# Kernel optimization log

Hardware: AMD Instinct MI355X
Metric: run time of the kernel (lower is better)

The kernel has to match this reference:

```python
import jax, jax.numpy as jnp
import numpy as np

B, T, Q, D = 8192, 65, 20, 100  # batch, tweet len, question len, 2*hidden_dim


def setup_inputs() -> dict:
    key = jax.random.key(0)
    kH, kU, k1, k2, k3 = jax.random.split(key, 5)
    # Ws params are a single normal row repeated across the length dim
    ws1 = jnp.tile(jax.random.normal(k1, (1, D), dtype=jnp.float32), (T, 1))
    ws2 = jnp.tile(jax.random.normal(k2, (1, D), dtype=jnp.float32), (Q, 1))
    ws3 = jnp.tile(jax.random.normal(k3, (1, D), dtype=jnp.float32), (T, 1))
    return {
        "H": jax.random.normal(kH, (B, T, D), dtype=jnp.float32),
        "U": jax.random.normal(kU, (B, Q, D), dtype=jnp.float32),
        "Ws1": ws1,
        "Ws2": ws2,
        "Ws3": ws3,
    }


def reference(H, U, Ws1, Ws2, Ws3):
    # H: [B,T,D], U: [B,Q,D]
    H1 = jnp.sum(H * Ws1, axis=2)[:, :, None]        # [B,T,1]
    U1 = jnp.sum(U * Ws2, axis=2)[:, None, :]        # [B,1,Q]
    HU = jnp.einsum('btd,bqd->btq', H * Ws3, U)      # [B,T,Q]
    S = H1 + U1 + HU                                 # [B,T,Q]
    at = jax.nn.softmax(S, axis=2)                   # attend tweet->question
    Util = jnp.einsum('btq,bqd->btd', at, U)         # [B,T,D]
    beta = jnp.max(S, axis=2)                        # [B,T]
    b = jax.nn.softmax(beta, axis=1)[:, :, None]     # [B,T,1]
    Htil = jnp.sum(b * H, axis=1)[:, None, :]        # [B,1,D] broadcast over T
    G = jnp.concatenate((H, Util, H * Util, H * Htil), axis=2)  # [B,T,4D]
    return G
```

## Files before the change

### kernel.cpp

```cpp
#include <hip/hip_runtime.h>
#include <math.h>

#define NB 8192
#define T 65
#define Q 20
#define D 100
#define D4 25
#define C 21
#define SP 24

__global__ __launch_bounds__(256) void attn_fused_kernel(
    const float* __restrict__ Hg,
    const float* __restrict__ Ug,
    const float* __restrict__ Ws1,
    const float* __restrict__ Ws2,
    const float* __restrict__ Ws3,
    float* __restrict__ Gg)
{
    __shared__ __align__(16) float sH[T*D];
    __shared__ __align__(16) float sU[Q*D];
    __shared__ __align__(16) float sU3e[C*D];
    __shared__ __align__(16) float sS[T*SP];
    __shared__ __align__(16) float sHtil[D];
    __shared__ float sU1q[Q];
    __shared__ float sBeta[T];
    __shared__ float sBsm[T];

    const int b   = blockIdx.x;
    const int tid = threadIdx.x;
    const float* Hb = Hg + (size_t)b * (T*D);
    const float* Ub = Ug + (size_t)b * (Q*D);
    float4* sH4   = (float4*)sH;
    float4* sU4   = (float4*)sU;
    float4* sU3e4 = (float4*)sU3e;
    float4* sS4   = (float4*)sS;

    {
        const float4* hs = (const float4*)Hb;
        for (int i = tid; i < T*D4; i += 256) sH4[i] = hs[i];
        const float4* us = (const float4*)Ub;
        for (int i = tid; i < Q*D4; i += 256) sU4[i] = us[i];
    }
    __syncthreads();

    {
        const float4* w3g = (const float4*)Ws3;
        const float4* w1g = (const float4*)Ws1;
        for (int i = tid; i < C*D4; i += 256) {
            const int r  = i / D4;
            const int dd = i - r*D4;
            float4 v;
            if (r < Q) {
                const float4 u = sU4[i];
                const float4 w = w3g[dd];
                v.x = u.x*w.x; v.y = u.y*w.y; v.z = u.z*w.z; v.w = u.w*w.w;
            } else {
                v = w1g[dd];
            }
            sU3e4[i] = v;
        }
        if (tid < Q) {
            const float4* ur = sU4 + tid*D4;
            const float4* w2 = (const float4*)Ws2;
            float acc = 0.f;
            #pragma unroll
            for (int k = 0; k < D4; ++k) {
                const float4 u = ur[k], w = w2[k];
                acc = fmaf(u.x, w.x, acc); acc = fmaf(u.y, w.y, acc);
                acc = fmaf(u.z, w.z, acc); acc = fmaf(u.w, w.w, acc);
            }
            sU1q[tid] = acc;
        }
    }
    __syncthreads();

    if (tid < 119) {
        const int tg = tid / 7;
        const int jg = tid - tg*7;
        const int t0 = tg*4;
        float acc[4][3];
        #pragma unroll
        for (int i = 0; i < 4; ++i)
            #pragma unroll
            for (int k = 0; k < 3; ++k) acc[i][k] = 0.f;
        #pragma unroll 5
        for (int d4 = 0; d4 < D4; ++d4) {
            float4 h[4];
            #pragma unroll
            for (int i = 0; i < 4; ++i) h[i] = sH4[(t0+i)*D4 + d4];
            #pragma unroll
            for (int k = 0; k < 3; ++k) {
                const float4 w = sU3e4[(jg*3+k)*D4 + d4];
                #pragma unroll
                for (int i = 0; i < 4; ++i) {
                    acc[i][k] = fmaf(h[i].x, w.x, acc[i][k]);
                    acc[i][k] = fmaf(h[i].y, w.y, acc[i][k]);
                    acc[i][k] = fmaf(h[i].z, w.z, acc[i][k]);
                    acc[i][k] = fmaf(h[i].w, w.w, acc[i][k]);
                }
            }
        }
        #pragma unroll
        for (int i = 0; i < 4; ++i) {
            const int t = t0 + i;
            if (t < T) {
                #pragma unroll
                for (int k = 0; k < 3; ++k) {
                    const int cc = jg*3 + k;
                    const float add = (cc < Q) ? sU1q[cc] : 0.f;
                    sS[t*SP + cc] = acc[i][k] + add;
                }
            }
        }
    }
    __syncthreads();

    if (tid < T) {
        const int t = tid;
        float4 r[5];
        #pragma unroll
        for (int c = 0; c < 5; ++c) r[c] = sS4[t*6 + c];
        const float h1t = sS[t*SP + 20];
        float m = r[0].x;
        #pragma unroll
        for (int c = 0; c < 5; ++c) {
            m = fmaxf(m, fmaxf(fmaxf(r[c].x, r[c].y), fmaxf(r[c].z, r[c].w)));
        }
        float s = 0.f;
        #pragma unroll
        for (int c = 0; c < 5; ++c) {
            r[c].x = __expf(r[c].x - m); r[c].y = __expf(r[c].y - m);
            r[c].z = __expf(r[c].z - m); r[c].w = __expf(r[c].w - m);
            s += r[c].x + r[c].y + r[c].z + r[c].w;
        }
        const float inv = 1.f / s;
        #pragma unroll
        for (int c = 0; c < 5; ++c) {
            r[c].x *= inv; r[c].y *= inv; r[c].z *= inv; r[c].w *= inv;
            sS4[t*6 + c] = r[c];
        }
        sBeta[t] = h1t + m;
    }
    __syncthreads();

    if (tid < 64) {
        const float v0 = sBeta[tid];
        const float v1 = (tid == 0) ? sBeta[64] : -1e30f;
        float mx = fmaxf(v0, v1);
        #pragma unroll
        for (int off = 32; off >= 1; off >>= 1)
            mx = fmaxf(mx, __shfl_xor(mx, off, 64));
        const float e0 = __expf(v0 - mx);
        const float e1 = (tid == 0) ? __expf(v1 - mx) : 0.f;
        float s = e0 + e1;
        #pragma unroll
        for (int off = 32; off >= 1; off >>= 1)
            s += __shfl_xor(s, off, 64);
        const float inv = 1.f / s;
        sBsm[tid] = e0 * inv;
        if (tid == 0) sBsm[64] = e1 * inv;
    }
    __syncthreads();

    if (tid < D4) {
        float4 acc = {0.f, 0.f, 0.f, 0.f};
        #pragma unroll 5
        for (int t = 0; t < T; ++t) {
            const float bt = sBsm[t];
            const float4 h = sH4[t*D4 + tid];
            acc.x = fmaf(bt, h.x, acc.x); acc.y = fmaf(bt, h.y, acc.y);
            acc.z = fmaf(bt, h.z, acc.z); acc.w = fmaf(bt, h.w, acc.w);
        }
        ((float4*)sHtil)[tid] = acc;
    }
    __syncthreads();

    {
        const int wv   = tid >> 6;
        const int lane = tid & 63;
        const int tsel = lane / 25;
        const int g    = lane - tsel*25;
        const bool act = (lane < 50);
        float* Gb = Gg + (size_t)b * (T*4*D);
        const float4 htil4 = ((float4*)sHtil)[g];
        const float4* ug = sU4 + g;

        for (int pr = wv; pr < 33; pr += 4) {
            const int t   = pr*2 + tsel;
            const bool val = act && (t < T);
            const int tr  = val ? t : 0;

            float4 a0 = sS4[tr*6 + 0];
            float4 a1 = sS4[tr*6 + 1];
            float4 a2 = sS4[tr*6 + 2];
            float4 a3 = sS4[tr*6 + 3];
            float4 a4 = sS4[tr*6 + 4];

            float4 acc = {0.f, 0.f, 0.f, 0.f};
            #define QSTEP(av, comp, qq) { \
                const float4 u = ug[(qq)*D4]; \
                acc.x = fmaf(av.comp, u.x, acc.x); \
                acc.y = fmaf(av.comp, u.y, acc.y); \
                acc.z = fmaf(av.comp, u.z, acc.z); \
                acc.w = fmaf(av.comp, u.w, acc.w); }
            QSTEP(a0,x,0)  QSTEP(a0,y,1)  QSTEP(a0,z,2)  QSTEP(a0,w,3)
            QSTEP(a1,x,4)  QSTEP(a1,y,5)  QSTEP(a1,z,6)  QSTEP(a1,w,7)
            QSTEP(a2,x,8)  QSTEP(a2,y,9)  QSTEP(a2,z,10) QSTEP(a2,w,11)
            QSTEP(a3,x,12) QSTEP(a3,y,13) QSTEP(a3,z,14) QSTEP(a3,w,15)
            QSTEP(a4,x,16) QSTEP(a4,y,17) QSTEP(a4,z,18) QSTEP(a4,w,19)
            #undef QSTEP

            const float4 h4 = sH4[tr*D4 + g];
            if (val) {
                float* base = Gb + (size_t)t*(4*D);
                float4 hu, hh;
                hu.x = h4.x*acc.x;   hu.y = h4.y*acc.y;   hu.z = h4.z*acc.z;   hu.w = h4.w*acc.w;
                hh.x = h4.x*htil4.x; hh.y = h4.y*htil4.y; hh.z = h4.z*htil4.z; hh.w = h4.w*htil4.w;
                ((float4*)(base        ))[g] = h4;
                ((float4*)(base +   D  ))[g] = acc;
                ((float4*)(base + 2*D  ))[g] = hu;
                ((float4*)(base + 3*D  ))[g] = hh;
            }
        }
    }
}

extern "C" void kernel_launch(void* const* d_in, const int* in_sizes, int n_in,
                              void* d_out, int out_size, void* d_ws, size_t ws_size,
                              hipStream_t stream) {
    const float* H   = (const float*)d_in[0];
    const float* U   = (const float*)d_in[1];
    const float* Ws1 = (const float*)d_in[2];
    const float* Ws2 = (const float*)d_in[3];
    const float* Ws3 = (const float*)d_in[4];
    float* G = (float*)d_out;
    hipLaunchKernelGGL(attn_fused_kernel, dim3(NB), dim3(256), 0, stream,
                       H, U, Ws1, Ws2, Ws3, G);
}
```

Before: 320.8 us.

## Retile S-GEMM and Util phases, split Htil across waves, fuse U loads

The per-thread tile in the score GEMM grows from 4x3 to 8x3, and the U1 dot products move onto a separate wave so they run alongside it. Htil is reduced with all four waves through partial sums. The Util phase handles three rows per thread so each U load is reused. The U copy and the Ws3 scaling are fused into one global pass, which removes one barrier, and launch bounds now request 3 blocks per CU. The larger tiles raise register pressure, and the occupancy hint could cause spills.

```diff
diff --git a/kernel.cpp b/kernel.cpp
--- a/kernel.cpp
+++ b/kernel.cpp
@@ -6,10 +6,9 @@
 #define Q 20
 #define D 100
 #define D4 25
-#define C 21
-#define SP 24
-
-__global__ __launch_bounds__(256) void attn_fused_kernel(
+#define SP4 5
+
+__global__ __launch_bounds__(256, 3) void attn_fused_kernel(
     const float* __restrict__ Hg,
     const float* __restrict__ Ug,
     const float* __restrict__ Ws1,
@@ -17,129 +16,122 @@
     const float* __restrict__ Ws3,
     float* __restrict__ Gg)
 {
-    __shared__ __align__(16) float sH[T*D];
-    __shared__ __align__(16) float sU[Q*D];
-    __shared__ __align__(16) float sU3e[C*D];
-    __shared__ __align__(16) float sS[T*SP];
-    __shared__ __align__(16) float sHtil[D];
-    __shared__ float sU1q[Q];
-    __shared__ float sBeta[T];
-    __shared__ float sBsm[T];
+    __shared__ float4 sH4[T*D4];
+    __shared__ float4 sU4[Q*D4];
+    __shared__ float4 sU3e4[(Q+1)*D4];
+    __shared__ float4 sS4[T*SP4];
+    __shared__ float4 sHtilP[4][D4];
+    __shared__ float4 sU1q4[SP4];
+    __shared__ float  sH1[T];
+    __shared__ float  sBeta[T];
+    __shared__ float  sBsm[T];
 
     const int b   = blockIdx.x;
     const int tid = threadIdx.x;
-    const float* Hb = Hg + (size_t)b * (T*D);
-    const float* Ub = Ug + (size_t)b * (Q*D);
-    float4* sH4   = (float4*)sH;
-    float4* sU4   = (float4*)sU;
-    float4* sU3e4 = (float4*)sU3e;
-    float4* sS4   = (float4*)sS;
-
-    {
-        const float4* hs = (const float4*)Hb;
-        for (int i = tid; i < T*D4; i += 256) sH4[i] = hs[i];
-        const float4* us = (const float4*)Ub;
-        for (int i = tid; i < Q*D4; i += 256) sU4[i] = us[i];
-    }
-    __syncthreads();
-
+    const float4* Hb = (const float4*)(Hg + (size_t)b * (T*D));
+    const float4* Ub = (const float4*)(Ug + (size_t)b * (Q*D));
+
+    for (int i = tid; i < T*D4; i += 256) sH4[i] = Hb[i];
     {
         const float4* w3g = (const float4*)Ws3;
-        const float4* w1g = (const float4*)Ws1;
-        for (int i = tid; i < C*D4; i += 256) {
-            const int r  = i / D4;
-            const int dd = i - r*D4;
-            float4 v;
-            if (r < Q) {
-                const float4 u = sU4[i];
-                const float4 w = w3g[dd];
-                v.x = u.x*w.x; v.y = u.y*w.y; v.z = u.z*w.z; v.w = u.w*w.w;
-            } else {
-                v = w1g[dd];
-            }
+        for (int i = tid; i < Q*D4; i += 256) {
+            const float4 u = Ub[i];
+            sU4[i] = u;
+            const int dd = i - (i/D4)*D4;
+            const float4 w = w3g[dd];
+            float4 v; v.x=u.x*w.x; v.y=u.y*w.y; v.z=u.z*w.z; v.w=u.w*w.w;
             sU3e4[i] = v;
         }
-        if (tid < Q) {
-            const float4* ur = sU4 + tid*D4;
-            const float4* w2 = (const float4*)Ws2;
-            float acc = 0.f;
-            #pragma unroll
-            for (int k = 0; k < D4; ++k) {
-                const float4 u = ur[k], w = w2[k];
-                acc = fmaf(u.x, w.x, acc); acc = fmaf(u.y, w.y, acc);
-                acc = fmaf(u.z, w.z, acc); acc = fmaf(u.w, w.w, acc);
-            }
-            sU1q[tid] = acc;
-        }
-    }
-    __syncthreads();
-
-    if (tid < 119) {
+        if (tid < D4) sU3e4[Q*D4 + tid] = ((const float4*)Ws1)[tid];
+    }
+    __syncthreads();
+
+    if (tid < 63) {
         const int tg = tid / 7;
         const int jg = tid - tg*7;
-        const int t0 = tg*4;
-        float acc[4][3];
-        #pragma unroll
-        for (int i = 0; i < 4; ++i)
+        int tb[8];
+        #pragma unroll
+        for (int i = 0; i < 8; ++i) {
+            const int t = tg*8 + i;
+            tb[i] = ((t < T) ? t : T-1) * D4;
+        }
+        float acc[8][3];
+        #pragma unroll
+        for (int i = 0; i < 8; ++i)
             #pragma unroll
             for (int k = 0; k < 3; ++k) acc[i][k] = 0.f;
         #pragma unroll 5
         for (int d4 = 0; d4 < D4; ++d4) {
-            float4 h[4];
-            #pragma unroll
-            for (int i = 0; i < 4; ++i) h[i] = sH4[(t0+i)*D4 + d4];
-            #pragma unroll
-            for (int k = 0; k < 3; ++k) {
-                const float4 w = sU3e4[(jg*3+k)*D4 + d4];
+            float4 w[3];
+            #pragma unroll
+            for (int k = 0; k < 3; ++k) w[k] = sU3e4[(jg*3+k)*D4 + d4];
+            #pragma unroll
+            for (int i = 0; i < 8; ++i) {
+                const float4 h = sH4[tb[i] + d4];
                 #pragma unroll
-                for (int i = 0; i < 4; ++i) {
-                    acc[i][k] = fmaf(h[i].x, w.x, acc[i][k]);
-                    acc[i][k] = fmaf(h[i].y, w.y, acc[i][k]);
-                    acc[i][k] = fmaf(h[i].z, w.z, acc[i][k]);
-                    acc[i][k] = fmaf(h[i].w, w.w, acc[i][k]);
+                for (int k = 0; k < 3; ++k) {
+                    acc[i][k] = fmaf(h.x, w[k].x, acc[i][k]);
+                    acc[i][k] = fmaf(h.y, w[k].y, acc[i][k]);
+                    acc[i][k] = fmaf(h.z, w[k].z, acc[i][k]);
+                    acc[i][k] = fmaf(h.w, w[k].w, acc[i][k]);
                 }
             }
         }
-        #pragma unroll
-        for (int i = 0; i < 4; ++i) {
-            const int t = t0 + i;
+        float* sSf = (float*)sS4;
+        #pragma unroll
+        for (int i = 0; i < 8; ++i) {
+            const int t = tg*8 + i;
             if (t < T) {
                 #pragma unroll
                 for (int k = 0; k < 3; ++k) {
                     const int cc = jg*3 + k;
-                    const float add = (cc < Q) ? sU1q[cc] : 0.f;
-                    sS[t*SP + cc] = acc[i][k] + add;
+                    if (cc < Q) sSf[t*(4*SP4) + cc] = acc[i][k];
+                    else        sH1[t] = acc[i][k];
                 }
             }
         }
+    } else if (tid >= 64 && tid < 64 + Q) {
+        const int q = tid - 64;
+        const float4* ur = sU4 + q*D4;
+        const float4* w2 = (const float4*)Ws2;
+        float acc = 0.f;
+        #pragma unroll
+        for (int k = 0; k < D4; ++k) {
+            const float4 u = ur[k], w = w2[k];
+            acc = fmaf(u.x, w.x, acc); acc = fmaf(u.y, w.y, acc);
+            acc = fmaf(u.z, w.z, acc); acc = fmaf(u.w, w.w, acc);
+        }
+        ((float*)sU1q4)[q] = acc;
     }
     __syncthreads();
 
     if (tid < T) {
         const int t = tid;
-        float4 r[5];
-        #pragma unroll
-        for (int c = 0; c < 5; ++c) r[c] = sS4[t*6 + c];
-        const float h1t = sS[t*SP + 20];
+        float4 r[SP4];
+        #pragma unroll
+        for (int c = 0; c < SP4; ++c) {
+            r[c] = sS4[t*SP4 + c];
+            const float4 u1 = sU1q4[c];
+            r[c].x += u1.x; r[c].y += u1.y; r[c].z += u1.z; r[c].w += u1.w;
+        }
         float m = r[0].x;
         #pragma unroll
-        for (int c = 0; c < 5; ++c) {
+        for (int c = 0; c < SP4; ++c)
             m = fmaxf(m, fmaxf(fmaxf(r[c].x, r[c].y), fmaxf(r[c].z, r[c].w)));
-        }
         float s = 0.f;
         #pragma unroll
-        for (int c = 0; c < 5; ++c) {
+        for (int c = 0; c < SP4; ++c) {
             r[c].x = __expf(r[c].x - m); r[c].y = __expf(r[c].y - m);
             r[c].z = __expf(r[c].z - m); r[c].w = __expf(r[c].w - m);
             s += r[c].x + r[c].y + r[c].z + r[c].w;
         }
         const float inv = 1.f / s;
         #pragma unroll
-        for (int c = 0; c < 5; ++c) {
+        for (int c = 0; c < SP4; ++c) {
             r[c].x *= inv; r[c].y *= inv; r[c].z *= inv; r[c].w *= inv;
-            sS4[t*6 + c] = r[c];
-        }
-        sBeta[t] = h1t + m;
+            sS4[t*SP4 + c] = r[c];
+        }
+        sBeta[t] = sH1[t] + m;
     }
     __syncthreads();
 
@@ -162,16 +154,18 @@
     }
     __syncthreads();
 
-    if (tid < D4) {
-        float4 acc = {0.f, 0.f, 0.f, 0.f};
-        #pragma unroll 5
-        for (int t = 0; t < T; ++t) {
-            const float bt = sBsm[t];
-            const float4 h = sH4[t*D4 + tid];
-            acc.x = fmaf(bt, h.x, acc.x); acc.y = fmaf(bt, h.y, acc.y);
-            acc.z = fmaf(bt, h.z, acc.z); acc.w = fmaf(bt, h.w, acc.w);
-        }
-        ((float4*)sHtil)[tid] = acc;
+    {
+        const int wv = tid >> 6, lane = tid & 63;
+        if (lane < D4) {
+            float4 acc = {0.f, 0.f, 0.f, 0.f};
+            for (int t = wv; t < T; t += 4) {
+                const float bt = sBsm[t];
+                const float4 h = sH4[t*D4 + lane];
+                acc.x = fmaf(bt, h.x, acc.x); acc.y = fmaf(bt, h.y, acc.y);
+                acc.z = fmaf(bt, h.z, acc.z); acc.w = fmaf(bt, h.w, acc.w);
+            }
+            sHtilP[wv][lane] = acc;
+        }
     }
     __syncthreads();
 
@@ -182,45 +176,62 @@
         const int g    = lane - tsel*25;
         const bool act = (lane < 50);
         float* Gb = Gg + (size_t)b * (T*4*D);
-        const float4 htil4 = ((float4*)sHtil)[g];
-        const float4* ug = sU4 + g;
-
-        for (int pr = wv; pr < 33; pr += 4) {
-            const int t   = pr*2 + tsel;
-            const bool val = act && (t < T);
-            const int tr  = val ? t : 0;
-
-            float4 a0 = sS4[tr*6 + 0];
-            float4 a1 = sS4[tr*6 + 1];
-            float4 a2 = sS4[tr*6 + 2];
-            float4 a3 = sS4[tr*6 + 3];
-            float4 a4 = sS4[tr*6 + 4];
-
-            float4 acc = {0.f, 0.f, 0.f, 0.f};
-            #define QSTEP(av, comp, qq) { \
-                const float4 u = ug[(qq)*D4]; \
-                acc.x = fmaf(av.comp, u.x, acc.x); \
-                acc.y = fmaf(av.comp, u.y, acc.y); \
-                acc.z = fmaf(av.comp, u.z, acc.z); \
-                acc.w = fmaf(av.comp, u.w, acc.w); }
-            QSTEP(a0,x,0)  QSTEP(a0,y,1)  QSTEP(a0,z,2)  QSTEP(a0,w,3)
-            QSTEP(a1,x,4)  QSTEP(a1,y,5)  QSTEP(a1,z,6)  QSTEP(a1,w,7)
-            QSTEP(a2,x,8)  QSTEP(a2,y,9)  QSTEP(a2,z,10) QSTEP(a2,w,11)
-            QSTEP(a3,x,12) QSTEP(a3,y,13) QSTEP(a3,z,14) QSTEP(a3,w,15)
-            QSTEP(a4,x,16) QSTEP(a4,y,17) QSTEP(a4,z,18) QSTEP(a4,w,19)
-            #undef QSTEP
-
-            const float4 h4 = sH4[tr*D4 + g];
-            if (val) {
-                float* base = Gb + (size_t)t*(4*D);
-                float4 hu, hh;
-                hu.x = h4.x*acc.x;   hu.y = h4.y*acc.y;   hu.z = h4.z*acc.z;   hu.w = h4.w*acc.w;
-                hh.x = h4.x*htil4.x; hh.y = h4.y*htil4.y; hh.z = h4.z*htil4.z; hh.w = h4.w*htil4.w;
-                ((float4*)(base        ))[g] = h4;
-                ((float4*)(base +   D  ))[g] = acc;
-                ((float4*)(base + 2*D  ))[g] = hu;
-                ((float4*)(base + 3*D  ))[g] = hh;
-            }
+
+        const float4 p0 = sHtilP[0][g], p1 = sHtilP[1][g], p2 = sHtilP[2][g], p3 = sHtilP[3][g];
+        float4 htil;
+        htil.x = p0.x+p1.x+p2.x+p3.x; htil.y = p0.y+p1.y+p2.y+p3.y;
+        htil.z = p0.z+p1.z+p2.z+p3.z; htil.w = p0.w+p1.w+p2.w+p3.w;
+
+        for (int c = wv; c < 11; c += 4) {
+            const int t0 = c*6 + tsel;
+            int tr0 = (t0     < T) ? t0     : T-1;
+            int tr1 = (t0 + 2 < T) ? t0 + 2 : T-1;
+            int tr2 = (t0 + 4 < T) ? t0 + 4 : T-1;
+            float4 a0[SP4], a1[SP4], a2[SP4];
+            #pragma unroll
+            for (int j = 0; j < SP4; ++j) {
+                a0[j] = sS4[tr0*SP4 + j];
+                a1[j] = sS4[tr1*SP4 + j];
+                a2[j] = sS4[tr2*SP4 + j];
+            }
+            float4 c0 = {0,0,0,0}, c1 = {0,0,0,0}, c2 = {0,0,0,0};
+            #define QST(qq, comp) { \
+                const float4 u = sU4[(qq)*D4 + g]; \
+                c0.x = fmaf(a0[(qq)>>2].comp, u.x, c0.x); \
+                c0.y = fmaf(a0[(qq)>>2].comp, u.y, c0.y); \
+                c0.z = fmaf(a0[(qq)>>2].comp, u.z, c0.z); \
+                c0.w = fmaf(a0[(qq)>>2].comp, u.w, c0.w); \
+                c1.x = fmaf(a1[(qq)>>2].comp, u.x, c1.x); \
+                c1.y = fmaf(a1[(qq)>>2].comp, u.y, c1.y); \
+                c1.z = fmaf(a1[(qq)>>2].comp, u.z, c1.z); \
+                c1.w = fmaf(a1[(qq)>>2].comp, u.w, c1.w); \
+                c2.x = fmaf(a2[(qq)>>2].comp, u.x, c2.x); \
+                c2.y = fmaf(a2[(qq)>>2].comp, u.y, c2.y); \
+                c2.z = fmaf(a2[(qq)>>2].comp, u.z, c2.z); \
+                c2.w = fmaf(a2[(qq)>>2].comp, u.w, c2.w); }
+            QST(0,x)  QST(1,y)  QST(2,z)  QST(3,w)
+            QST(4,x)  QST(5,y)  QST(6,z)  QST(7,w)
+            QST(8,x)  QST(9,y)  QST(10,z) QST(11,w)
+            QST(12,x) QST(13,y) QST(14,z) QST(15,w)
+            QST(16,x) QST(17,y) QST(18,z) QST(19,w)
+            #undef QST
+
+            #define PSTORE(p, cacc) { \
+                const int t = t0 + 2*(p); \
+                if (act && t < T) { \
+                    const float4 hv = sH4[t*D4 + g]; \
+                    float4 hu, hh; \
+                    hu.x = hv.x*(cacc).x; hu.y = hv.y*(cacc).y; hu.z = hv.z*(cacc).z; hu.w = hv.w*(cacc).w; \
+                    hh.x = hv.x*htil.x;   hh.y = hv.y*htil.y;   hh.z = hv.z*htil.z;   hh.w = hv.w*htil.w; \
+                    float4* base = (float4*)(Gb + (size_t)t*(4*D)); \
+                    base[g]        = hv; \
+                    base[D4 + g]   = (cacc); \
+                    base[2*D4 + g] = hu; \
+                    base[3*D4 + g] = hh; } }
+            PSTORE(0, c0)
+            PSTORE(1, c1)
+            PSTORE(2, c2)
+            #undef PSTORE
         }
     }
 }
```

Result: slower. 399.1 us (+24.4%).
